# Performance work log

Hardware: AMD Instinct MI355X
Metric: run time of the kernel (lower is better)

## Reference

```python
import jax, jax.numpy as jnp
import numpy as np

N_NODES = 50000
N_EDGES = 800000
DIM = 64
N_ETYPES = 4
N_STEPS = 5


def setup_inputs() -> dict:
    key = jax.random.key(0)
    ks = jax.random.split(key, 10)
    feat = jax.random.normal(ks[0], (N_NODES, DIM), dtype=jnp.float32)
    src = jax.random.randint(ks[1], (N_EDGES,), 0, N_NODES, dtype=jnp.int32)
    dst = jax.random.randint(ks[2], (N_EDGES,), 0, N_NODES, dtype=jnp.int32)
    etypes = jax.random.randint(ks[3], (N_EDGES,), 0, N_ETYPES, dtype=jnp.int32)
    # per-edge-type Linear weights, xavier_normal with relu gain, zero bias
    gain = float(np.sqrt(2.0))
    std = gain * float(np.sqrt(2.0 / (DIM + DIM)))
    W = jax.random.normal(ks[4], (N_ETYPES, DIM, DIM), dtype=jnp.float32) * std  # [T, out, in]
    b = jnp.zeros((N_ETYPES, DIM), dtype=jnp.float32)
    # GRUCell params (torch layout: [3*dim, dim], gates order r,z,n), uniform(-1/sqrt(dim), 1/sqrt(dim))
    bound = 1.0 / float(np.sqrt(DIM))
    w_ih = jax.random.uniform(ks[5], (3 * DIM, DIM), minval=-bound, maxval=bound, dtype=jnp.float32)
    w_hh = jax.random.uniform(ks[6], (3 * DIM, DIM), minval=-bound, maxval=bound, dtype=jnp.float32)
    b_ih = jax.random.uniform(ks[7], (3 * DIM,), minval=-bound, maxval=bound, dtype=jnp.float32)
    b_hh = jax.random.uniform(ks[8], (3 * DIM,), minval=-bound, maxval=bound, dtype=jnp.float32)
    return {"feat": feat, "W": W, "b": b, "w_ih": w_ih, "w_hh": w_hh,
            "b_ih": b_ih, "b_hh": b_hh, "src": src, "dst": dst, "etypes": etypes}


def _gru_cell(a, h, w_ih, w_hh, b_ih, b_hh):
    gi = a @ w_ih.T + b_ih  # [N, 3*D]
    gh = h @ w_hh.T + b_hh
    i_r, i_z, i_n = jnp.split(gi, 3, axis=-1)
    h_r, h_z, h_n = jnp.split(gh, 3, axis=-1)
    r = jax.nn.sigmoid(i_r + h_r)
    z = jax.nn.sigmoid(i_z + h_z)
    n = jnp.tanh(i_n + r * h_n)
    return (1.0 - z) * n + z * h


def reference(feat, W, b, w_ih, w_hh, b_ih, b_hh, src, dst, etypes):
    n_nodes = feat.shape[0]
    h = feat
    for _ in range(N_STEPS):
        # apply every etype linear to all nodes: [N, T, D]
        h_all = jnp.einsum('nd,ted->nte', h, W) + b
        # per-edge message selects src node under its edge type: [E, D]
        m = h_all[src, etypes]
        # scatter-sum to destination nodes: [N, D]
        a = jax.ops.segment_sum(m, dst, num_segments=n_nodes)
        h = _gru_cell(a, h, w_ih, w_hh, b_ih, b_hh)
    return h
```

## Files before the change

### kernel.cpp

```cpp
#include <hip/hip_runtime.h>
#include <hip/hip_bf16.h>
#include <cstdint>

#define DIM 64
#define TD 256
#define NSTEPS 5
#define HS  68
#define GLDH 194
#define MAXDEG 48

typedef __attribute__((ext_vector_type(8))) short short8v;
typedef __attribute__((ext_vector_type(4))) float f32x4;
typedef __attribute__((ext_vector_type(8))) _Float16 half8v;

__device__ __forceinline__ float fast_sigmoid(float x){
  return 1.0f / (1.0f + __expf(-x));
}
__device__ __forceinline__ float fast_tanh(float x){
  return 2.0f / (1.0f + __expf(-2.0f * x)) - 1.0f;
}

__device__ __forceinline__ unsigned short f2bf(float x){
  unsigned u = __builtin_bit_cast(unsigned, x);
  return (unsigned short)((u + 0x7FFFu + ((u>>16)&1u)) >> 16);
}
__device__ __forceinline__ float bf2f(unsigned short b){
  unsigned u = ((unsigned)b)<<16;
  return __builtin_bit_cast(float, u);
}

__device__ __forceinline__ void splitbf8(const float* __restrict__ p,
                                         short8v& hi, short8v& lo){
  float4 x0 = *(const float4*)p;
  float4 x1 = *(const float4*)(p+4);
  float xs[8] = {x0.x,x0.y,x0.z,x0.w,x1.x,x1.y,x1.z,x1.w};
#pragma unroll
  for(int i=0;i<8;i++){
    unsigned short hb = f2bf(xs[i]);
    float rem = xs[i] - bf2f(hb);
    hi[i] = (short)hb;
    lo[i] = (short)f2bf(rem);
  }
}

__global__ __launch_bounds__(256) void k_pack(const float* __restrict__ src,
    short* __restrict__ ph, short* __restrict__ pl, int ncoltiles, int mode){
  int idx = blockIdx.x*256 + threadIdx.x;
  int total = ncoltiles*1024;
  if (idx >= total) return;
  int e = idx & 7, lane = (idx>>3)&63, kc = (idx>>9)&1, ct = idx>>10;
  int col = ct*16 + (lane&15);
  int k = kc*32 + (lane>>4)*8 + e;
  float v;
  if (mode==0){ int t = col>>6, eo = col&63; v = src[(size_t)(t*64+eo)*64 + k]; }
  else        { v = src[(size_t)col*64 + k]; }
  unsigned short hb = f2bf(v);
  float rem = v - bf2f(hb);
  ph[idx] = (short)hb;
  pl[idx] = (short)f2bf(rem);
}

__global__ __launch_bounds__(256) void k_transform_mfma(
    const float* __restrict__ h, const short* __restrict__ pth,
    const short* __restrict__ ptl, const float* __restrict__ b,
    _Float16* __restrict__ h_all, int n_nodes){
  const int wave = threadIdx.x >> 6, lane = threadIdx.x & 63;
  const int n0 = blockIdx.x * 16;
  if (n0 >= n_nodes) return;
  const int arow = n0 + (lane & 15);
  const int kb = (lane >> 4) * 8;
  short8v ah0,al0,ah1,al1;
  splitbf8(h + (size_t)arow*DIM + kb,      ah0, al0);
  splitbf8(h + (size_t)arow*DIM + 32 + kb, ah1, al1);
  const int crow = n0 + (lane >> 4) * 4;
  const int cc = lane & 15;
#pragma unroll
  for (int i = 0; i < 4; ++i){
    int ct = wave*4 + i;
    const short8v bh0 = *(const short8v*)(pth + ((size_t)(ct*2+0)*64 + lane)*8);
    const short8v bh1 = *(const short8v*)(pth + ((size_t)(ct*2+1)*64 + lane)*8);
    const short8v bl0 = *(const short8v*)(ptl + ((size_t)(ct*2+0)*64 + lane)*8);
    const short8v bl1 = *(const short8v*)(ptl + ((size_t)(ct*2+1)*64 + lane)*8);
    float bias = b[ct*16 + cc];
    f32x4 acc = {bias,bias,bias,bias};
    acc = __builtin_amdgcn_mfma_f32_16x16x32_bf16(ah0, bh0, acc, 0,0,0);
    acc = __builtin_amdgcn_mfma_f32_16x16x32_bf16(ah1, bh1, acc, 0,0,0);
    acc = __builtin_amdgcn_mfma_f32_16x16x32_bf16(al0, bh0, acc, 0,0,0);
    acc = __builtin_amdgcn_mfma_f32_16x16x32_bf16(al1, bh1, acc, 0,0,0);
    acc = __builtin_amdgcn_mfma_f32_16x16x32_bf16(ah0, bl0, acc, 0,0,0);
    acc = __builtin_amdgcn_mfma_f32_16x16x32_bf16(ah1, bl1, acc, 0,0,0);
#pragma unroll
    for (int q=0;q<4;q++)
      h_all[(size_t)(crow + q)*TD + ct*16 + cc] = (_Float16)acc[q];
  }
}

__global__ __launch_bounds__(256) void k_scatter_ell(
    const int* __restrict__ src, const int* __restrict__ dst,
    const int* __restrict__ et, int* __restrict__ deg,
    int* __restrict__ ell, int n_edges) {
  int e = blockIdx.x * 256 + threadIdx.x;
  if (e >= n_edges) return;
  int d0 = dst[e];
  int rank = atomicAdd(&deg[d0], 1);
  if (rank < MAXDEG)
    ell[(size_t)d0 * MAXDEG + rank] = (src[e] << 2) | et[e];
}

__global__ __launch_bounds__(256) void k_step(
    const _Float16* __restrict__ h_in, _Float16* __restrict__ h_out,
    const int* __restrict__ ell, const int* __restrict__ deg,
    float* __restrict__ h,
    const short* __restrict__ pih_h, const short* __restrict__ pih_l,
    const short* __restrict__ phh_h, const short* __restrict__ phh_l,
    const float* __restrict__ b_ih, const float* __restrict__ b_hh,
    const short* __restrict__ pth, const short* __restrict__ ptl,
    const float* __restrict__ bb,
    int n_nodes, int do_transform){
  __shared__ __align__(16) char smem[4352 + 12416];
  float (*atile)[HS] = (float(*)[HS])smem;
  float (*hnew)[HS]  = (float(*)[HS])smem;
  _Float16* gbuf     = (_Float16*)(smem + 4352);

  const int tid = threadIdx.x;
  const int wave = tid >> 6, lane = tid & 63;
  const int n0 = blockIdx.x * 16;
  if (n0 >= n_nodes) return;

  {
    int j = tid >> 4;
    int q = tid & 15;
    int eslot = q >> 3;
    int dimg = q & 7;
    int node = n0 + j;
    int dg = min(deg[node], MAXDEG);
    const int* eb = ell + (size_t)node * MAXDEG;
    float acc[8] = {0,0,0,0,0,0,0,0};
    int i = eslot;
    for (; i + 6 < dg; i += 8) {
      int p0 = eb[i], p1 = eb[i+2], p2 = eb[i+4], p3 = eb[i+6];
      half8v v0 = *(const half8v*)(h_in + (size_t)(p0>>2)*TD + (p0&3)*DIM + dimg*8);
      half8v v1 = *(const half8v*)(h_in + (size_t)(p1>>2)*TD + (p1&3)*DIM + dimg*8);
      half8v v2 = *(const half8v*)(h_in + (size_t)(p2>>2)*TD + (p2&3)*DIM + dimg*8);
      half8v v3 = *(const half8v*)(h_in + (size_t)(p3>>2)*TD + (p3&3)*DIM + dimg*8);
#pragma unroll
      for (int k=0;k<8;k++)
        acc[k] += ((float)v0[k] + (float)v1[k]) + ((float)v2[k] + (float)v3[k]);
    }
    for (; i < dg; i += 2) {
      int p0 = eb[i];
      half8v v0 = *(const half8v*)(h_in + (size_t)(p0>>2)*TD + (p0&3)*DIM + dimg*8);
#pragma unroll
      for (int k=0;k<8;k++) acc[k] += (float)v0[k];
    }
#pragma unroll
    for (int k=0;k<8;k++) acc[k] += __shfl_xor(acc[k], 8);
    if (eslot == 0) {
#pragma unroll
      for (int k=0;k<8;k++) atile[j][dimg*8+k] = acc[k];
    }
  }
  __syncthreads();

  const bool is_h = wave >= 2;
  const short* __restrict__ pbh = is_h ? phh_h : pih_h;
  const short* __restrict__ pbl = is_h ? phh_l : pih_l;
  const float* __restrict__ bv  = is_h ? b_hh : b_ih;
  _Float16* outb = gbuf + (is_h ? 16*GLDH : 0);

  const int kb = (lane >> 4) * 8;
  short8v ah0,al0,ah1,al1;
  if (is_h) {
    const float* xp = h + (size_t)(n0 + (lane & 15))*DIM;
    splitbf8(xp + kb,      ah0, al0);
    splitbf8(xp + 32 + kb, ah1, al1);
  } else {
    const float* xp = &atile[lane & 15][0];
    splitbf8(xp + kb,      ah0, al0);
    splitbf8(xp + 32 + kb, ah1, al1);
  }

  const int ct0 = (wave & 1) * 6;
  const int rr = (lane >> 4) * 4;
  const int cc = lane & 15;
#pragma unroll
  for (int i = 0; i < 6; ++i){
    int ct = ct0 + i;
    const short8v bh0 = *(const short8v*)(pbh + ((size_t)(ct*2+0)*64 + lane)*8);
    const short8v bh1 = *(const short8v*)(pbh + ((size_t)(ct*2+1)*64 + lane)*8);
    const short8v bl0 = *(const short8v*)(pbl + ((size_t)(ct*2+0)*64 + lane)*8);
    const short8v bl1 = *(const short8v*)(pbl + ((size_t)(ct*2+1)*64 + lane)*8);
    float bias = bv[ct*16 + cc];
    f32x4 acc = {bias,bias,bias,bias};
    acc = __builtin_amdgcn_mfma_f32_16x16x32_bf16(ah0, bh0, acc, 0,0,0);
    acc = __builtin_amdgcn_mfma_f32_16x16x32_bf16(ah1, bh1, acc, 0,0,0);
    acc = __builtin_amdgcn_mfma_f32_16x16x32_bf16(al0, bh0, acc, 0,0,0);
    acc = __builtin_amdgcn_mfma_f32_16x16x32_bf16(al1, bh1, acc, 0,0,0);
    acc = __builtin_amdgcn_mfma_f32_16x16x32_bf16(ah0, bl0, acc, 0,0,0);
    acc = __builtin_amdgcn_mfma_f32_16x16x32_bf16(ah1, bl1, acc, 0,0,0);
#pragma unroll
    for (int q=0;q<4;q++)
      outb[(rr+q)*GLDH + ct*16 + cc] = (_Float16)acc[q];
  }
  __syncthreads();

#pragma unroll
  for (int it=0; it<4; ++it){
    int t = it*256 + tid;
    int j = t >> 6, d = t & 63;
    float gir = (float)gbuf[j*GLDH + d];
    float giz = (float)gbuf[j*GLDH + 64 + d];
    float gin = (float)gbuf[j*GLDH + 128 + d];
    float ghr = (float)gbuf[16*GLDH + j*GLDH + d];
    float ghz = (float)gbuf[16*GLDH + j*GLDH + 64 + d];
    float ghn = (float)gbuf[16*GLDH + j*GLDH + 128 + d];
    float r  = fast_sigmoid(gir + ghr);
    float z  = fast_sigmoid(giz + ghz);
    float nv = fast_tanh   (gin + r*ghn);
    size_t off = (size_t)(n0+j)*DIM + d;
    float ho = h[off];
    float hn = (1.0f - z)*nv + z*ho;
    h[off] = hn;
    hnew[j][d] = hn;
  }
  if (!do_transform) return;
  __syncthreads();

  short8v th0,tl0,th1,tl1;
  splitbf8(&hnew[lane & 15][kb],      th0, tl0);
  splitbf8(&hnew[lane & 15][32 + kb], th1, tl1);
  const int crow = n0 + (lane >> 4) * 4;
#pragma unroll
  for (int i = 0; i < 4; ++i){
    int ct = wave*4 + i;
    const short8v bh0 = *(const short8v*)(pth + ((size_t)(ct*2+0)*64 + lane)*8);
    const short8v bh1 = *(const short8v*)(pth + ((size_t)(ct*2+1)*64 + lane)*8);
    const short8v bl0 = *(const short8v*)(ptl + ((size_t)(ct*2+0)*64 + lane)*8);
    const short8v bl1 = *(const short8v*)(ptl + ((size_t)(ct*2+1)*64 + lane)*8);
    float bias = bb[ct*16 + cc];
    f32x4 acc = {bias,bias,bias,bias};
    acc = __builtin_amdgcn_mfma_f32_16x16x32_bf16(th0, bh0, acc, 0,0,0);
    acc = __builtin_amdgcn_mfma_f32_16x16x32_bf16(th1, bh1, acc, 0,0,0);
    acc = __builtin_amdgcn_mfma_f32_16x16x32_bf16(tl0, bh0, acc, 0,0,0);
    acc = __builtin_amdgcn_mfma_f32_16x16x32_bf16(tl1, bh1, acc, 0,0,0);
    acc = __builtin_amdgcn_mfma_f32_16x16x32_bf16(th0, bl0, acc, 0,0,0);
    acc = __builtin_amdgcn_mfma_f32_16x16x32_bf16(th1, bl1, acc, 0,0,0);
#pragma unroll
    for (int q=0;q<4;q++)
      h_out[(size_t)(crow + q)*TD + ct*16 + cc] = (_Float16)acc[q];
  }
}

extern "C" void kernel_launch(void* const* d_in, const int* in_sizes, int n_in,
                              void* d_out, int out_size, void* d_ws, size_t ws_size,
                              hipStream_t stream) {
  const float* feat = (const float*)d_in[0];
  const float* W    = (const float*)d_in[1];
  const float* b    = (const float*)d_in[2];
  const float* w_ih = (const float*)d_in[3];
  const float* w_hh = (const float*)d_in[4];
  const float* b_ih = (const float*)d_in[5];
  const float* b_hh = (const float*)d_in[6];
  const int* src = (const int*)d_in[7];
  const int* dst = (const int*)d_in[8];
  const int* et  = (const int*)d_in[9];

  const int n_nodes = in_sizes[0] / DIM;
  const int n_edges = in_sizes[7];

  float* h = (float*)d_out;
  char* ws = (char*)d_ws;
  _Float16* hall0 = (_Float16*)ws;  ws += (size_t)n_nodes * TD * sizeof(_Float16);
  _Float16* hall1 = (_Float16*)ws;  ws += (size_t)n_nodes * TD * sizeof(_Float16);
  int* ell     = (int*)ws;      ws += (size_t)n_nodes * MAXDEG * sizeof(int);
  int* deg     = (int*)ws;      ws += (size_t)n_nodes * sizeof(int);
  short* pt_h  = (short*)ws;    ws += 16384 * sizeof(short);
  short* pt_l  = (short*)ws;    ws += 16384 * sizeof(short);
  short* pih_h = (short*)ws;    ws += 12288 * sizeof(short);
  short* pih_l = (short*)ws;    ws += 12288 * sizeof(short);
  short* phh_h = (short*)ws;    ws += 12288 * sizeof(short);
  short* phh_l = (short*)ws;    ws += 12288 * sizeof(short);

  hipMemcpyAsync(h, feat, (size_t)n_nodes * DIM * sizeof(float),
                 hipMemcpyDeviceToDevice, stream);

  k_pack<<<64, 256, 0, stream>>>(W,    pt_h,  pt_l,  16, 0);
  k_pack<<<48, 256, 0, stream>>>(w_ih, pih_h, pih_l, 12, 1);
  k_pack<<<48, 256, 0, stream>>>(w_hh, phh_h, phh_l, 12, 1);

  const int nblk_edges = (n_edges + 255) / 256;
  hipMemsetAsync(deg, 0, (size_t)n_nodes * sizeof(int), stream);
  k_scatter_ell<<<nblk_edges, 256, 0, stream>>>(src, dst, et, deg, ell, n_edges);

  const int rtiles = (n_nodes + 15) / 16;

  k_transform_mfma<<<rtiles, 256, 0, stream>>>(h, pt_h, pt_l, b, hall0, n_nodes);
  for (int s = 0; s < NSTEPS; ++s) {
    const _Float16* hin = (s & 1) ? hall1 : hall0;
    _Float16* hout      = (s & 1) ? hall0 : hall1;
    k_step<<<rtiles, 256, 0, stream>>>(hin, hout, ell, deg, h,
                                       pih_h, pih_l, phh_h, phh_l, b_ih, b_hh,
                                       pt_h, pt_l, b, n_nodes,
                                       (s < NSTEPS - 1) ? 1 : 0);
  }
}
```

Before: 320.3 us.

## Keep hidden state in fp16 and use f16 MFMA with split weights

The hidden state is now stored as an fp16 copy instead of fp32. The hidden-side GEMMs (the W_hh gates and the per-etype transform) use f16 MFMA on an unsplit fp16 activation against split hi/lo fp16 weights, which cuts six MFMAs to four per tile and removes the activation splitting. The fp32 output is written only on the last step, and the initial device copy is replaced by a cast kernel. This reduces memory traffic and instruction count, but the recurrent state is rounded to fp16 each step, which may lose accuracy over five steps.

```diff
diff --git a/kernel.cpp b/kernel.cpp
--- a/kernel.cpp
+++ b/kernel.cpp
@@ -6,6 +6,7 @@
 #define TD 256
 #define NSTEPS 5
 #define HS  68
+#define HHS 72
 #define GLDH 194
 #define MAXDEG 48
 
@@ -44,7 +45,21 @@
 }
 
 __global__ __launch_bounds__(256) void k_pack(const float* __restrict__ src,
-    short* __restrict__ ph, short* __restrict__ pl, int ncoltiles, int mode){
+    short* __restrict__ ph, short* __restrict__ pl, int ncoltiles){
+  int idx = blockIdx.x*256 + threadIdx.x;
+  int total = ncoltiles*1024;
+  if (idx >= total) return;
+  int e = idx & 7, lane = (idx>>3)&63, kc = (idx>>9)&1, ct = idx>>10;
+  int col = ct*16 + (lane&15);
+  int k = kc*32 + (lane>>4)*8 + e;
+  float v = src[(size_t)col*64 + k];
+  unsigned short hb = f2bf(v);
+  ph[idx] = (short)hb;
+  pl[idx] = (short)f2bf(v - bf2f(hb));
+}
+
+__global__ __launch_bounds__(256) void k_packh(const float* __restrict__ src,
+    _Float16* __restrict__ ph, _Float16* __restrict__ pl, int ncoltiles, int mode){
   int idx = blockIdx.x*256 + threadIdx.x;
   int total = ncoltiles*1024;
   if (idx >= total) return;
@@ -54,45 +69,18 @@
   float v;
   if (mode==0){ int t = col>>6, eo = col&63; v = src[(size_t)(t*64+eo)*64 + k]; }
   else        { v = src[(size_t)col*64 + k]; }
-  unsigned short hb = f2bf(v);
-  float rem = v - bf2f(hb);
-  ph[idx] = (short)hb;
-  pl[idx] = (short)f2bf(rem);
-}
-
-__global__ __launch_bounds__(256) void k_transform_mfma(
-    const float* __restrict__ h, const short* __restrict__ pth,
-    const short* __restrict__ ptl, const float* __restrict__ b,
-    _Float16* __restrict__ h_all, int n_nodes){
-  const int wave = threadIdx.x >> 6, lane = threadIdx.x & 63;
-  const int n0 = blockIdx.x * 16;
-  if (n0 >= n_nodes) return;
-  const int arow = n0 + (lane & 15);
-  const int kb = (lane >> 4) * 8;
-  short8v ah0,al0,ah1,al1;
-  splitbf8(h + (size_t)arow*DIM + kb,      ah0, al0);
-  splitbf8(h + (size_t)arow*DIM + 32 + kb, ah1, al1);
-  const int crow = n0 + (lane >> 4) * 4;
-  const int cc = lane & 15;
-#pragma unroll
-  for (int i = 0; i < 4; ++i){
-    int ct = wave*4 + i;
-    const short8v bh0 = *(const short8v*)(pth + ((size_t)(ct*2+0)*64 + lane)*8);
-    const short8v bh1 = *(const short8v*)(pth + ((size_t)(ct*2+1)*64 + lane)*8);
-    const short8v bl0 = *(const short8v*)(ptl + ((size_t)(ct*2+0)*64 + lane)*8);
-    const short8v bl1 = *(const short8v*)(ptl + ((size_t)(ct*2+1)*64 + lane)*8);
-    float bias = b[ct*16 + cc];
-    f32x4 acc = {bias,bias,bias,bias};
-    acc = __builtin_amdgcn_mfma_f32_16x16x32_bf16(ah0, bh0, acc, 0,0,0);
-    acc = __builtin_amdgcn_mfma_f32_16x16x32_bf16(ah1, bh1, acc, 0,0,0);
-    acc = __builtin_amdgcn_mfma_f32_16x16x32_bf16(al0, bh0, acc, 0,0,0);
-    acc = __builtin_amdgcn_mfma_f32_16x16x32_bf16(al1, bh1, acc, 0,0,0);
-    acc = __builtin_amdgcn_mfma_f32_16x16x32_bf16(ah0, bl0, acc, 0,0,0);
-    acc = __builtin_amdgcn_mfma_f32_16x16x32_bf16(ah1, bl1, acc, 0,0,0);
-#pragma unroll
-    for (int q=0;q<4;q++)
-      h_all[(size_t)(crow + q)*TD + ct*16 + cc] = (_Float16)acc[q];
-  }
+  _Float16 hv = (_Float16)v;
+  ph[idx] = hv;
+  pl[idx] = (_Float16)(v - (float)hv);
+}
+
+__global__ __launch_bounds__(256) void k_cast(const float* __restrict__ x,
+                                              _Float16* __restrict__ y, int n4){
+  int i = blockIdx.x*256 + threadIdx.x;
+  if (i >= n4) return;
+  float4 v = *(const float4*)(x + (size_t)i*4);
+  y[(size_t)i*4+0] = (_Float16)v.x; y[(size_t)i*4+1] = (_Float16)v.y;
+  y[(size_t)i*4+2] = (_Float16)v.z; y[(size_t)i*4+3] = (_Float16)v.w;
 }
 
 __global__ __launch_bounds__(256) void k_scatter_ell(
@@ -107,20 +95,52 @@
     ell[(size_t)d0 * MAXDEG + rank] = (src[e] << 2) | et[e];
 }
 
+__global__ __launch_bounds__(256) void k_transform_mfma(
+    const _Float16* __restrict__ hb, const _Float16* __restrict__ pth,
+    const _Float16* __restrict__ ptl, const float* __restrict__ b,
+    _Float16* __restrict__ h_all, int n_nodes){
+  const int wave = threadIdx.x >> 6, lane = threadIdx.x & 63;
+  const int n0 = blockIdx.x * 16;
+  if (n0 >= n_nodes) return;
+  const int arow = n0 + (lane & 15);
+  const int kb = (lane >> 4) * 8;
+  half8v ah0 = *(const half8v*)(hb + (size_t)arow*DIM + kb);
+  half8v ah1 = *(const half8v*)(hb + (size_t)arow*DIM + 32 + kb);
+  const int crow = n0 + (lane >> 4) * 4;
+  const int cc = lane & 15;
+#pragma unroll
+  for (int i = 0; i < 4; ++i){
+    int ct = wave*4 + i;
+    const half8v bh0 = *(const half8v*)(pth + ((size_t)(ct*2+0)*64 + lane)*8);
+    const half8v bh1 = *(const half8v*)(pth + ((size_t)(ct*2+1)*64 + lane)*8);
+    const half8v bl0 = *(const half8v*)(ptl + ((size_t)(ct*2+0)*64 + lane)*8);
+    const half8v bl1 = *(const half8v*)(ptl + ((size_t)(ct*2+1)*64 + lane)*8);
+    float bias = b[ct*16 + cc];
+    f32x4 acc = {bias,bias,bias,bias};
+    acc = __builtin_amdgcn_mfma_f32_16x16x32_f16(ah0, bh0, acc, 0,0,0);
+    acc = __builtin_amdgcn_mfma_f32_16x16x32_f16(ah1, bh1, acc, 0,0,0);
+    acc = __builtin_amdgcn_mfma_f32_16x16x32_f16(ah0, bl0, acc, 0,0,0);
+    acc = __builtin_amdgcn_mfma_f32_16x16x32_f16(ah1, bl1, acc, 0,0,0);
+#pragma unroll
+    for (int q=0;q<4;q++)
+      h_all[(size_t)(crow + q)*TD + ct*16 + cc] = (_Float16)acc[q];
+  }
+}
+
 __global__ __launch_bounds__(256) void k_step(
     const _Float16* __restrict__ h_in, _Float16* __restrict__ h_out,
     const int* __restrict__ ell, const int* __restrict__ deg,
-    float* __restrict__ h,
+    _Float16* __restrict__ hb, float* __restrict__ hfull,
     const short* __restrict__ pih_h, const short* __restrict__ pih_l,
-    const short* __restrict__ phh_h, const short* __restrict__ phh_l,
+    const _Float16* __restrict__ phh_h, const _Float16* __restrict__ phh_l,
     const float* __restrict__ b_ih, const float* __restrict__ b_hh,
-    const short* __restrict__ pth, const short* __restrict__ ptl,
+    const _Float16* __restrict__ pth, const _Float16* __restrict__ ptl,
     const float* __restrict__ bb,
-    int n_nodes, int do_transform){
+    int n_nodes, int do_transform, int write_out){
   __shared__ __align__(16) char smem[4352 + 12416];
-  float (*atile)[HS] = (float(*)[HS])smem;
-  float (*hnew)[HS]  = (float(*)[HS])smem;
-  _Float16* gbuf     = (_Float16*)(smem + 4352);
+  float    (*atile)[HS]  = (float(*)[HS])smem;
+  _Float16 (*hnewh)[HHS] = (_Float16(*)[HHS])smem;
+  _Float16* gbuf         = (_Float16*)(smem + 4352);
 
   const int tid = threadIdx.x;
   const int wave = tid >> 6, lane = tid & 63;
@@ -162,45 +182,58 @@
   }
   __syncthreads();
 
-  const bool is_h = wave >= 2;
-  const short* __restrict__ pbh = is_h ? phh_h : pih_h;
-  const short* __restrict__ pbl = is_h ? phh_l : pih_l;
-  const float* __restrict__ bv  = is_h ? b_hh : b_ih;
-  _Float16* outb = gbuf + (is_h ? 16*GLDH : 0);
-
   const int kb = (lane >> 4) * 8;
-  short8v ah0,al0,ah1,al1;
-  if (is_h) {
-    const float* xp = h + (size_t)(n0 + (lane & 15))*DIM;
+  const int rr = (lane >> 4) * 4;
+  const int cc = lane & 15;
+
+  if (wave < 2) {
+    const float* xp = &atile[lane & 15][0];
+    short8v ah0,al0,ah1,al1;
     splitbf8(xp + kb,      ah0, al0);
     splitbf8(xp + 32 + kb, ah1, al1);
+    const int ct0 = (wave & 1) * 6;
+#pragma unroll
+    for (int i = 0; i < 6; ++i){
+      int ct = ct0 + i;
+      const short8v bh0 = *(const short8v*)(pih_h + ((size_t)(ct*2+0)*64 + lane)*8);
+      const short8v bh1 = *(const short8v*)(pih_h + ((size_t)(ct*2+1)*64 + lane)*8);
+      const short8v bl0 = *(const short8v*)(pih_l + ((size_t)(ct*2+0)*64 + lane)*8);
+      const short8v bl1 = *(const short8v*)(pih_l + ((size_t)(ct*2+1)*64 + lane)*8);
+      float bias = b_ih[ct*16 + cc];
+      f32x4 acc = {bias,bias,bias,bias};
+      acc = __builtin_amdgcn_mfma_f32_16x16x32_bf16(ah0, bh0, acc, 0,0,0);
+      acc = __builtin_amdgcn_mfma_f32_16x16x32_bf16(ah1, bh1, acc, 0,0,0);
+      acc = __builtin_amdgcn_mfma_f32_16x16x32_bf16(al0, bh0, acc, 0,0,0);
+      acc = __builtin_amdgcn_mfma_f32_16x16x32_bf16(al1, bh1, acc, 0,0,0);
+      acc = __builtin_amdgcn_mfma_f32_16x16x32_bf16(ah0, bl0, acc, 0,0,0);
+      acc = __builtin_amdgcn_mfma_f32_16x16x32_bf16(ah1, bl1, acc, 0,0,0);
+#pragma unroll
+      for (int q=0;q<4;q++)
+        gbuf[(rr+q)*GLDH + ct*16 + cc] = (_Float16)acc[q];
+    }
   } else {
-    const float* xp = &atile[lane & 15][0];
-    splitbf8(xp + kb,      ah0, al0);
-    splitbf8(xp + 32 + kb, ah1, al1);
-  }
-
-  const int ct0 = (wave & 1) * 6;
-  const int rr = (lane >> 4) * 4;
-  const int cc = lane & 15;
-#pragma unroll
-  for (int i = 0; i < 6; ++i){
-    int ct = ct0 + i;
-    const short8v bh0 = *(const short8v*)(pbh + ((size_t)(ct*2+0)*64 + lane)*8);
-    const short8v bh1 = *(const short8v*)(pbh + ((size_t)(ct*2+1)*64 + lane)*8);
-    const short8v bl0 = *(const short8v*)(pbl + ((size_t)(ct*2+0)*64 + lane)*8);
-    const short8v bl1 = *(const short8v*)(pbl + ((size_t)(ct*2+1)*64 + lane)*8);
-    float bias = bv[ct*16 + cc];
-    f32x4 acc = {bias,bias,bias,bias};
-    acc = __builtin_amdgcn_mfma_f32_16x16x32_bf16(ah0, bh0, acc, 0,0,0);
-    acc = __builtin_amdgcn_mfma_f32_16x16x32_bf16(ah1, bh1, acc, 0,0,0);
-    acc = __builtin_amdgcn_mfma_f32_16x16x32_bf16(al0, bh0, acc, 0,0,0);
-    acc = __builtin_amdgcn_mfma_f32_16x16x32_bf16(al1, bh1, acc, 0,0,0);
-    acc = __builtin_amdgcn_mfma_f32_16x16x32_bf16(ah0, bl0, acc, 0,0,0);
-    acc = __builtin_amdgcn_mfma_f32_16x16x32_bf16(ah1, bl1, acc, 0,0,0);
-#pragma unroll
-    for (int q=0;q<4;q++)
-      outb[(rr+q)*GLDH + ct*16 + cc] = (_Float16)acc[q];
+    _Float16* outb = gbuf + 16*GLDH;
+    const _Float16* xp = hb + (size_t)(n0 + (lane & 15))*DIM;
+    half8v ah0 = *(const half8v*)(xp + kb);
+    half8v ah1 = *(const half8v*)(xp + 32 + kb);
+    const int ct0 = (wave & 1) * 6;
+#pragma unroll
+    for (int i = 0; i < 6; ++i){
+      int ct = ct0 + i;
+      const half8v bh0 = *(const half8v*)(phh_h + ((size_t)(ct*2+0)*64 + lane)*8);
+      const half8v bh1 = *(const half8v*)(phh_h + ((size_t)(ct*2+1)*64 + lane)*8);
+      const half8v bl0 = *(const half8v*)(phh_l + ((size_t)(ct*2+0)*64 + lane)*8);
+      const half8v bl1 = *(const half8v*)(phh_l + ((size_t)(ct*2+1)*64 + lane)*8);
+      float bias = b_hh[ct*16 + cc];
+      f32x4 acc = {bias,bias,bias,bias};
+      acc = __builtin_amdgcn_mfma_f32_16x16x32_f16(ah0, bh0, acc, 0,0,0);
+      acc = __builtin_amdgcn_mfma_f32_16x16x32_f16(ah1, bh1, acc, 0,0,0);
+      acc = __builtin_amdgcn_mfma_f32_16x16x32_f16(ah0, bl0, acc, 0,0,0);
+      acc = __builtin_amdgcn_mfma_f32_16x16x32_f16(ah1, bl1, acc, 0,0,0);
+#pragma unroll
+      for (int q=0;q<4;q++)
+        outb[(rr+q)*GLDH + ct*16 + cc] = (_Float16)acc[q];
+    }
   }
   __syncthreads();
 
@@ -218,33 +251,32 @@
     float z  = fast_sigmoid(giz + ghz);
     float nv = fast_tanh   (gin + r*ghn);
     size_t off = (size_t)(n0+j)*DIM + d;
-    float ho = h[off];
+    float ho = (float)hb[off];
     float hn = (1.0f - z)*nv + z*ho;
-    h[off] = hn;
-    hnew[j][d] = hn;
+    _Float16 hq = (_Float16)hn;
+    hb[off] = hq;
+    if (write_out) hfull[off] = hn;
+    hnewh[j][d] = hq;
   }
   if (!do_transform) return;
   __syncthreads();
 
-  short8v th0,tl0,th1,tl1;
-  splitbf8(&hnew[lane & 15][kb],      th0, tl0);
-  splitbf8(&hnew[lane & 15][32 + kb], th1, tl1);
+  half8v th0 = *(const half8v*)(&hnewh[lane & 15][kb]);
+  half8v th1 = *(const half8v*)(&hnewh[lane & 15][32 + kb]);
   const int crow = n0 + (lane >> 4) * 4;
 #pragma unroll
   for (int i = 0; i < 4; ++i){
     int ct = wave*4 + i;
-    const short8v bh0 = *(const short8v*)(pth + ((size_t)(ct*2+0)*64 + lane)*8);
-    const short8v bh1 = *(const short8v*)(pth + ((size_t)(ct*2+1)*64 + lane)*8);
-    const short8v bl0 = *(const short8v*)(ptl + ((size_t)(ct*2+0)*64 + lane)*8);
-    const short8v bl1 = *(const short8v*)(ptl + ((size_t)(ct*2+1)*64 + lane)*8);
+    const half8v bh0 = *(const half8v*)(pth + ((size_t)(ct*2+0)*64 + lane)*8);
+    const half8v bh1 = *(const half8v*)(pth + ((size_t)(ct*2+1)*64 + lane)*8);
+    const half8v bl0 = *(const half8v*)(ptl + ((size_t)(ct*2+0)*64 + lane)*8);
+    const half8v bl1 = *(const half8v*)(ptl + ((size_t)(ct*2+1)*64 + lane)*8);
     float bias = bb[ct*16 + cc];
     f32x4 acc = {bias,bias,bias,bias};
-    acc = __builtin_amdgcn_mfma_f32_16x16x32_bf16(th0, bh0, acc, 0,0,0);
-    acc = __builtin_amdgcn_mfma_f32_16x16x32_bf16(th1, bh1, acc, 0,0,0);
-    acc = __builtin_amdgcn_mfma_f32_16x16x32_bf16(tl0, bh0, acc, 0,0,0);
-    acc = __builtin_amdgcn_mfma_f32_16x16x32_bf16(tl1, bh1, acc, 0,0,0);
-    acc = __builtin_amdgcn_mfma_f32_16x16x32_bf16(th0, bl0, acc, 0,0,0);
-    acc = __builtin_amdgcn_mfma_f32_16x16x32_bf16(th1, bl1, acc, 0,0,0);
+    acc = __builtin_amdgcn_mfma_f32_16x16x32_f16(th0, bh0, acc, 0,0,0);
+    acc = __builtin_amdgcn_mfma_f32_16x16x32_f16(th1, bh1, acc, 0,0,0);
+    acc = __builtin_amdgcn_mfma_f32_16x16x32_f16(th0, bl0, acc, 0,0,0);
+    acc = __builtin_amdgcn_mfma_f32_16x16x32_f16(th1, bl1, acc, 0,0,0);
 #pragma unroll
     for (int q=0;q<4;q++)
       h_out[(size_t)(crow + q)*TD + ct*16 + cc] = (_Float16)acc[q];
@@ -268,25 +300,24 @@
   const int n_nodes = in_sizes[0] / DIM;
   const int n_edges = in_sizes[7];
 
-  float* h = (float*)d_out;
+  float* hfull = (float*)d_out;
   char* ws = (char*)d_ws;
   _Float16* hall0 = (_Float16*)ws;  ws += (size_t)n_nodes * TD * sizeof(_Float16);
   _Float16* hall1 = (_Float16*)ws;  ws += (size_t)n_nodes * TD * sizeof(_Float16);
+  _Float16* hb    = (_Float16*)ws;  ws += (size_t)n_nodes * DIM * sizeof(_Float16);
   int* ell     = (int*)ws;      ws += (size_t)n_nodes * MAXDEG * sizeof(int);
   int* deg     = (int*)ws;      ws += (size_t)n_nodes * sizeof(int);
-  short* pt_h  = (short*)ws;    ws += 16384 * sizeof(short);
-  short* pt_l  = (short*)ws;    ws += 16384 * sizeof(short);
+  _Float16* pt_h  = (_Float16*)ws;  ws += 16384 * sizeof(_Float16);
+  _Float16* pt_l  = (_Float16*)ws;  ws += 16384 * sizeof(_Float16);
   short* pih_h = (short*)ws;    ws += 12288 * sizeof(short);
   short* pih_l = (short*)ws;    ws += 12288 * sizeof(short);
-  short* phh_h = (short*)ws;    ws += 12288 * sizeof(short);
-  short* phh_l = (short*)ws;    ws += 12288 * sizeof(short);
-
-  hipMemcpyAsync(h, feat, (size_t)n_nodes * DIM * sizeof(float),
-                 hipMemcpyDeviceToDevice, stream);
-
-  k_pack<<<64, 256, 0, stream>>>(W,    pt_h,  pt_l,  16, 0);
-  k_pack<<<48, 256, 0, stream>>>(w_ih, pih_h, pih_l, 12, 1);
-  k_pack<<<48, 256, 0, stream>>>(w_hh, phh_h, phh_l, 12, 1);
+  _Float16* phh_h = (_Float16*)ws;  ws += 12288 * sizeof(_Float16);
+  _Float16* phh_l = (_Float16*)ws;  ws += 12288 * sizeof(_Float16);
+
+  k_packh<<<64, 256, 0, stream>>>(W,    pt_h,  pt_l,  16, 0);
+  k_pack <<<48, 256, 0, stream>>>(w_ih, pih_h, pih_l, 12);
+  k_packh<<<48, 256, 0, stream>>>(w_hh, phh_h, phh_l, 12, 1);
+  k_cast<<<(n_nodes*DIM/4 + 255)/256, 256, 0, stream>>>(feat, hb, n_nodes*DIM/4);
 
   const int nblk_edges = (n_edges + 255) / 256;
   hipMemsetAsync(deg, 0, (size_t)n_nodes * sizeof(int), stream);
@@ -294,13 +325,14 @@
 
   const int rtiles = (n_nodes + 15) / 16;
 
-  k_transform_mfma<<<rtiles, 256, 0, stream>>>(h, pt_h, pt_l, b, hall0, n_nodes);
+  k_transform_mfma<<<rtiles, 256, 0, stream>>>(hb, pt_h, pt_l, b, hall0, n_nodes);
   for (int s = 0; s < NSTEPS; ++s) {
     const _Float16* hin = (s & 1) ? hall1 : hall0;
     _Float16* hout      = (s & 1) ? hall0 : hall1;
-    k_step<<<rtiles, 256, 0, stream>>>(hin, hout, ell, deg, h,
+    k_step<<<rtiles, 256, 0, stream>>>(hin, hout, ell, deg, hb, hfull,
                                        pih_h, pih_l, phh_h, phh_l, b_ih, b_hh,
                                        pt_h, pt_l, b, n_nodes,
-                                       (s < NSTEPS - 1) ? 1 : 0);
-  }
-}
+                                       (s < NSTEPS - 1) ? 1 : 0,
+                                       (s == NSTEPS - 1) ? 1 : 0);
+  }
+}
```

After: 297.4 us. 1.08x faster.
